# Kernel tuning notes

Measured on AMD Instinct MI355X. Metric: run time of the kernel, lower is better.

Reference implementation:

```python
import jax, jax.numpy as jnp
import numpy as np

NB_CLS, NB_QRY, NB_SHOT, FEAT_DIM = 5, 75, 5, 640
Q_STEPS, LR_DNI, HID = 3, 1e-3, 4096
N = NB_CLS + NB_QRY           # nodes in similarity graph (80)
M = 1 + N                     # subgraph size (81)
# strict upper triangle of MxM minus the query-query block (matches triu_index_input)
_t = np.ones((M, M)); _t[1 + NB_CLS:, 1 + NB_CLS:] = 0
_t = np.triu(_t, 1)
MASK_IDX = jnp.asarray(np.flatnonzero(_t.ravel() == 1))
DNI_IN = int(MASK_IDX.shape[0])  # 465


def _pairwise(supp, query):
    feat = jnp.concatenate([supp, query], 0)
    nrm = jnp.maximum(jnp.linalg.norm(feat, axis=-1, keepdims=True), 1e-12)
    feat = feat / nrm
    sim = feat @ feat.T                      # (N, N)
    sim_ss = sim[:NB_CLS, :NB_CLS]
    sim_qq = sim[NB_CLS:, NB_CLS:]
    sim_sq = sim[:NB_CLS, NB_CLS:]
    sim_feat_support = jnp.concatenate([sim_ss, sim_sq], 1).T   # (N, nb_cls)
    sim_feat_query = jnp.concatenate([sim_sq, sim_qq], 0)       # (N, nb_qry)
    return sim_feat_support, sim_feat_query, sim_sq


def _subgraph(sim_s, sim_q):
    # topk indices are constants wrt grad (no_grad in torch; ints in jax)
    idx_q = jax.lax.top_k(sim_q, NB_QRY)[1] + NB_CLS
    idx_s = jax.lax.top_k(sim_s, NB_CLS)[1]
    index = jnp.concatenate([jnp.arange(N, dtype=idx_s.dtype)[:, None], idx_s, idx_q], 1)  # (N, M)
    sim = jnp.concatenate([sim_s, sim_q], 1)                     # (N, N)
    sub = sim[index[:, :, None], index[:, None, :]]              # (N, M, M) batched gather
    return sub.reshape(N, M * M)[:, MASK_IDX]                    # (N, DNI_IN)


def _dni(x, W1, b1, W2, b2, W3, b3):
    h = jax.nn.relu(x @ W1.T + b1)
    h = jax.nn.relu(h @ W2.T + b2)
    return h @ W3.T + b3


def _refine(supp, query, ds, dq):
    for _ in range(Q_STEPS):
        inputs, vjp = jax.vjp(lambda s: _subgraph(*_pairwise(s, query)[:2]), supp)
        supp = supp - LR_DNI * vjp(_dni(inputs, *ds))[0]
        inputs, vjp = jax.vjp(lambda q: _subgraph(*_pairwise(supp, q)[:2]), query)
        query = query - LR_DNI * vjp(_dni(inputs, *dq))[0]
    return supp, query


def setup_inputs() -> dict:
    key = jax.random.key(0)
    ks = jax.random.split(key, 16)
    d = {
        "feat_support": jax.random.normal(ks[0], (NB_CLS, NB_SHOT, FEAT_DIM), jnp.float32),
        "feat_query": jax.random.normal(ks[1], (NB_QRY, FEAT_DIM), jnp.float32),
        "scale_cls": jnp.full((1,), 10.0, jnp.float32),
    }
    names = ["ds_W1", "ds_b1", "ds_W2", "ds_b2", "ds_W3", "ds_b3",
             "dq_W1", "dq_b1", "dq_W2", "dq_b2", "dq_W3", "dq_b3"]
    shapes = [(HID, DNI_IN), (HID,), (HID, HID), (HID,), (DNI_IN, HID), (DNI_IN,)] * 2
    for i, (n, sh) in enumerate(zip(names, shapes)):
        d[n] = jax.random.normal(ks[2 + i], sh, jnp.float32) * 0.02
    return d


def reference(feat_support, feat_query, scale_cls,
              ds_W1, ds_b1, ds_W2, ds_b2, ds_W3, ds_b3,
              dq_W1, dq_b1, dq_W2, dq_b2, dq_W3, dq_b3):
    supp = feat_support.mean(1)                                  # (nb_cls, feat_dim)
    ds = (ds_W1, ds_b1, ds_W2, ds_b2, ds_W3, ds_b3)
    dq = (dq_W1, dq_b1, dq_W2, dq_b2, dq_W3, dq_b3)
    supp, query = _refine(supp, feat_query, ds, dq)
    _, _, sim_sq = _pairwise(supp, query)
    return (sim_sq * scale_cls).T                                # (nb_qry, nb_cls)
```

## Files before the change

kernel.cpp:

```cpp
#include <hip/hip_runtime.h>

#define NCLS 5
#define NQRY 75
#define NTOT 80
#define FD   640
#define HIDN 4096
#define DNIN 465
#define KPAD 512
#define NPAD 512
#define LRDNI 1e-3f

#define KS1 4
#define KS2 16
#define KS3 32

typedef short  v8s __attribute__((ext_vector_type(8)));
typedef float  v4f __attribute__((ext_vector_type(4)));

__device__ __forceinline__ ushort f2bf(float x) {
    uint u = __float_as_uint(x);
    u = (u + 0x7FFFu + ((u >> 16) & 1u)) >> 16;
    return (ushort)u;
}
__device__ __forceinline__ uint pk2(float a, float b) {
    return (uint)f2bf(a) | ((uint)f2bf(b) << 16);
}

__global__ void k_init(const float* __restrict__ fs, const float* __restrict__ fq,
                       float* __restrict__ supp, float* __restrict__ qbuf) {
    int idx = blockIdx.x * 256 + threadIdx.x;
    if (idx < NCLS * FD) {
        int c = idx / FD, d = idx % FD;
        float s = 0.f;
        #pragma unroll
        for (int t = 0; t < 5; t++) s += fs[(c * 5 + t) * FD + d];
        supp[idx] = s * 0.2f;
    }
    if (idx < NQRY * FD) qbuf[idx] = fq[idx];
}

__global__ void k_cvtW1(const float* __restrict__ W, ushort* __restrict__ Wb) {
    int idx = blockIdx.x * 256 + threadIdx.x;
    int r = idx >> 9, c = idx & 511;
    Wb[idx] = (c < DNIN) ? f2bf(W[r * DNIN + c]) : (ushort)0;
}
__global__ void k_cvtW3(const float* __restrict__ W, ushort* __restrict__ Wb) {
    int idx = blockIdx.x * 256 + threadIdx.x;
    int r = idx >> 12;
    Wb[idx] = (r < DNIN) ? f2bf(W[idx]) : (ushort)0;
}

__device__ __forceinline__ const float* rowptr(const float* supp, const float* qbuf, int r) {
    return (r < NCLS) ? (supp + r * FD) : (qbuf + (r - NCLS) * FD);
}

template<bool FIN>
__global__ void k_simrank(const float* __restrict__ supp, const float* __restrict__ qbuf,
                          float* __restrict__ f, float* __restrict__ nrm,
                          float* __restrict__ S, int* __restrict__ perm,
                          const float* __restrict__ scale, float* __restrict__ out) {
    __shared__ float fi[FD];
    __shared__ float row[NTOT];
    __shared__ float ssh[NTOT];
    int i = blockIdx.x;
    int t = threadIdx.x;
    const float* ri = rowptr(supp, qbuf, i);
    for (int u = t; u < FD; u += 128) fi[u] = ri[u];
    __syncthreads();
    float dot = 0.f;
    if (t < NTOT) {
        const float* rj = rowptr(supp, qbuf, t);
        float ss = 0.f;
        for (int k = 0; k < FD; k += 4) {
            float4 a = *(const float4*)(fi + k);
            float4 b = *(const float4*)(rj + k);
            dot += a.x * b.x + a.y * b.y + a.z * b.z + a.w * b.w;
            ss  += b.x * b.x + b.y * b.y + b.z * b.z + b.w * b.w;
        }
        ssh[t] = ss;
    }
    __syncthreads();
    float ni = fmaxf(sqrtf(ssh[i]), 1e-12f);
    float inv_i = 1.0f / ni;
    if (t < NTOT) {
        float nt = fmaxf(sqrtf(ssh[t]), 1e-12f);
        float val = dot * inv_i / nt;
        if (FIN) {
            if (t >= NCLS) out[(t - NCLS) * NCLS + i] = val * scale[0];
        } else {
            row[t] = val;
            S[i * NTOT + t] = val;
        }
    }
    if (FIN) return;
    __syncthreads();
    for (int u = t; u < FD; u += 128) f[i * FD + u] = fi[u] * inv_i;
    if (t == 0) { nrm[i] = ni; perm[i * 81] = i; }
    if (t < NCLS) {
        float v = row[t]; int rank = 0;
        for (int k = 0; k < NCLS; k++) {
            float w = row[k];
            if (w > v || (w == v && k < t)) rank++;
        }
        perm[i * 81 + 1 + rank] = t;
    } else if (t < NTOT) {
        int j = t - NCLS; float v = row[t]; int rank = 0;
        for (int k = NCLS; k < NTOT; k++) {
            float w = row[k];
            if (w > v || (w == v && (k - NCLS) < j)) rank++;
        }
        perm[i * 81 + 6 + rank] = t;
    }
}

__device__ __forceinline__ void mask_ab(int m, int& a, int& b) {
    int start = 0, len = 80, aa = 0;
    while (m >= start + len) { start += len; len--; aa++; }
    a = aa; b = aa + 1 + (m - start);
}

__global__ void k_gather(const float* __restrict__ S, const int* __restrict__ perm,
                         ushort* __restrict__ Xb, float* __restrict__ Gs) {
    __shared__ int p[81];
    int i = blockIdx.x;
    int t = threadIdx.x;
    if (t < 81) p[t] = perm[i * 81 + t];
    if (t < NTOT) Gs[i * NTOT + t] = 0.f;
    __syncthreads();
    if (t < DNIN) {
        int a, b; mask_ab(t, a, b);
        Xb[i * KPAD + t] = f2bf(S[p[a] * NTOT + p[b]]);
    } else if (t < KPAD) {
        Xb[i * KPAD + t] = 0;
    }
}

template<int NT, bool BF32>
__global__ __launch_bounds__(256) void k_gemm(
        const ushort* __restrict__ A, int lda,
        const void* __restrict__ Bv, int ldb,
        float* __restrict__ C, int ldc, int kiters) {
    const int NB = NT * 64;
    __shared__ ushort As[80][68];
    __shared__ ushort Bs[NB][68];
    int tid = threadIdx.x;
    int w = tid >> 6, lane = tid & 63, l16 = lane & 15, quad = lane >> 4;
    int n00 = blockIdx.x * NB;
    int ks = blockIdx.y;
    int kc0 = ks * kiters * 64;

    v4f acc[5][NT];
    #pragma unroll
    for (int mt = 0; mt < 5; mt++)
        #pragma unroll
        for (int nt = 0; nt < NT; nt++) acc[mt][nt] = (v4f){0.f, 0.f, 0.f, 0.f};

    for (int it = 0; it < kiters; it++) {
        int k0 = kc0 + it * 64;
        for (int o = tid; o < 640; o += 256) {
            int r = o >> 3, c8 = o & 7;
            *(uint4*)&As[r][c8 * 8] = *(const uint4*)(A + r * lda + k0 + c8 * 8);
        }
        if (BF32) {
            const float* B = (const float*)Bv;
            #pragma unroll
            for (int o = tid; o < NB * 8; o += 256) {
                int r = o >> 3, c8 = o & 7;
                const float* p = B + (size_t)(n00 + r) * ldb + k0 + c8 * 8;
                float4 f0 = *(const float4*)p;
                float4 f1 = *(const float4*)(p + 4);
                uint4 q;
                q.x = pk2(f0.x, f0.y); q.y = pk2(f0.z, f0.w);
                q.z = pk2(f1.x, f1.y); q.w = pk2(f1.z, f1.w);
                *(uint4*)&Bs[r][c8 * 8] = q;
            }
        } else {
            const ushort* B = (const ushort*)Bv;
            #pragma unroll
            for (int o = tid; o < NB * 8; o += 256) {
                int r = o >> 3, c8 = o & 7;
                *(uint4*)&Bs[r][c8 * 8] = *(const uint4*)((const ushort*)B + (size_t)(n00 + r) * ldb + k0 + c8 * 8);
            }
        }
        __syncthreads();
        #pragma unroll
        for (int kb = 0; kb < 2; kb++) {
            int ko = kb * 32 + quad * 8;
            v8s bf[NT];
            #pragma unroll
            for (int nt = 0; nt < NT; nt++)
                bf[nt] = *(const v8s*)&Bs[w * NT * 16 + nt * 16 + l16][ko];
            #pragma unroll
            for (int mt = 0; mt < 5; mt++) {
                v8s af = *(const v8s*)&As[mt * 16 + l16][ko];
                #pragma unroll
                for (int nt = 0; nt < NT; nt++)
                    acc[mt][nt] = __builtin_amdgcn_mfma_f32_16x16x32_bf16(af, bf[nt], acc[mt][nt], 0, 0, 0);
            }
        }
        __syncthreads();
    }
    float* Cp = C + (size_t)ks * 80 * ldc;
    #pragma unroll
    for (int nt = 0; nt < NT; nt++) {
        int col = n00 + w * NT * 16 + nt * 16 + l16;
        #pragma unroll
        for (int mt = 0; mt < 5; mt++)
            #pragma unroll
            for (int r = 0; r < 4; r++)
                Cp[(mt * 16 + quad * 4 + r) * ldc + col] = acc[mt][nt][r];
    }
}

template<int NS>
__global__ void k_ep(const float* __restrict__ P, const float* __restrict__ bias,
                     ushort* __restrict__ H) {
    int idx = blockIdx.x * 256 + threadIdx.x;
    float s = bias[idx & 4095];
    #pragma unroll
    for (int ks = 0; ks < NS; ks++) s += P[ks * (80 * HIDN) + idx];
    H[idx] = f2bf(fmaxf(s, 0.f));
}

__global__ void k_scatter(const float* __restrict__ P3, const float* __restrict__ b3,
                          const int* __restrict__ perm, float* __restrict__ Gs) {
    __shared__ int p[81];
    int i = blockIdx.x;
    int t = threadIdx.x;
    if (t < 81) p[t] = perm[i * 81 + t];
    __syncthreads();
    if (t < DNIN) {
        float g = b3[t];
        #pragma unroll
        for (int ks = 0; ks < KS3; ks++) g += P3[ks * (80 * NPAD) + i * NPAD + t];
        int a, b; mask_ab(t, a, b);
        atomicAdd(&Gs[p[a] * NTOT + p[b]], g);
    }
}

__global__ void k_bwd(const float* __restrict__ Gs, const float* __restrict__ f,
                      const float* __restrict__ nrm, float* __restrict__ target,
                      int row0) {
    int r = row0 + blockIdx.x;
    __shared__ float cj[NTOT];
    __shared__ float red[2];
    int t = threadIdx.x;
    if (t < NTOT) cj[t] = Gs[r * NTOT + t] + Gs[t * NTOT + r];
    __syncthreads();
    float df[5] = {0.f, 0.f, 0.f, 0.f, 0.f};
    for (int j = 0; j < NTOT; j++) {
        float c = cj[j];
        const float* fj = f + j * FD;
        #pragma unroll
        for (int u = 0; u < 5; u++) df[u] += c * fj[t + 128 * u];
    }
    const float* fr = f + r * FD;
    float frv[5]; float partial = 0.f;
    #pragma unroll
    for (int u = 0; u < 5; u++) { frv[u] = fr[t + 128 * u]; partial += df[u] * frv[u]; }
    #pragma unroll
    for (int o = 32; o > 0; o >>= 1) partial += __shfl_xor(partial, o, 64);
    if ((t & 63) == 0) red[t >> 6] = partial;
    __syncthreads();
    float dot = red[0] + red[1];
    float invn = 1.0f / nrm[r];
    float* dst = target + blockIdx.x * FD;
    #pragma unroll
    for (int u = 0; u < 5; u++) {
        float dx = (df[u] - dot * frv[u]) * invn;
        dst[t + 128 * u] -= LRDNI * dx;
    }
}

extern "C" void kernel_launch(void* const* d_in, const int* in_sizes, int n_in,
                              void* d_out, int out_size, void* d_ws, size_t ws_size,
                              hipStream_t stream) {
    const float* fs    = (const float*)d_in[0];
    const float* fq    = (const float*)d_in[1];
    const float* scale = (const float*)d_in[2];
    const float* W[12];
    for (int i = 0; i < 12; i++) W[i] = (const float*)d_in[3 + i];

    float* base = (float*)d_ws;
    float* supp = base;
    float* qbuf = supp + 3200;
    float* f    = qbuf + 48000;
    float* nrm  = f + 51200;
    float* S    = nrm + 96;
    int*   perm = (int*)(S + 6400);
    float* P1   = (float*)(perm + 6496);
    float* P2   = P1 + (size_t)KS1 * 80 * HIDN;
    float* P3   = P2 + (size_t)KS2 * 80 * HIDN;
    float* Gs   = P3 + (size_t)KS3 * 80 * NPAD;
    ushort* Xb  = (ushort*)(Gs + 6400);
    ushort* H1b = Xb + 80 * KPAD;
    ushort* H2b = H1b + 80 * HIDN;
    ushort* W1b_ds = H2b + 80 * HIDN;
    ushort* W1b_dq = W1b_ds + HIDN * KPAD;
    ushort* W3b_ds = W1b_dq + HIDN * KPAD;
    ushort* W3b_dq = W3b_ds + NPAD * HIDN;

    k_cvtW1<<<8192, 256, 0, stream>>>(W[0],  W1b_ds);
    k_cvtW1<<<8192, 256, 0, stream>>>(W[6],  W1b_dq);
    k_cvtW3<<<8192, 256, 0, stream>>>(W[4],  W3b_ds);
    k_cvtW3<<<8192, 256, 0, stream>>>(W[10], W3b_dq);
    k_init<<<188, 256, 0, stream>>>(fs, fq, supp, qbuf);

    for (int step = 0; step < 3; step++) {
        for (int half = 0; half < 2; half++) {
            const float* const* w = (half == 0) ? W : (W + 6);
            const ushort* W1b = (half == 0) ? W1b_ds : W1b_dq;
            const ushort* W3b = (half == 0) ? W3b_ds : W3b_dq;
            k_simrank<false><<<80, 128, 0, stream>>>(supp, qbuf, f, nrm, S, perm, nullptr, nullptr);
            k_gather<<<80, 512, 0, stream>>>(S, perm, Xb, Gs);
            k_gemm<1, false><<<dim3(64, KS1), 256, 0, stream>>>(
                Xb, KPAD, W1b, KPAD, P1, HIDN, 2);
            k_ep<KS1><<<1280, 256, 0, stream>>>(P1, w[1], H1b);
            k_gemm<2, true><<<dim3(32, KS2), 256, 0, stream>>>(
                H1b, HIDN, w[2], HIDN, P2, HIDN, 4);
            k_ep<KS2><<<1280, 256, 0, stream>>>(P2, w[3], H2b);
            k_gemm<1, false><<<dim3(8, KS3), 256, 0, stream>>>(
                H2b, HIDN, W3b, HIDN, P3, NPAD, 2);
            k_scatter<<<80, 512, 0, stream>>>(P3, w[5], perm, Gs);
            if (half == 0) k_bwd<<<5, 128, 0, stream>>>(Gs, f, nrm, supp, 0);
            else           k_bwd<<<75, 128, 0, stream>>>(Gs, f, nrm, qbuf, NCLS);
        }
    }
    k_simrank<true><<<5, 128, 0, stream>>>(supp, qbuf, f, nrm, S, perm, scale, (float*)d_out);
}
```

Before: 654.6 us.

## Pre-convert W2 to bf16, load GEMM fragments directly, vectorize epilogue

Converts the two 4096x4096 W2 matrices to bf16 once up front, which halves the bytes the middle GEMM reads from memory on each of its six uses. The GEMM drops shared-memory staging and barriers, and each wave now loads its MFMA fragments straight from global memory. Layer 1 uses a wider K split (8 instead of 4). The bias+ReLU epilogue is vectorized to float4 loads. The cost is extra one-time conversion work and workspace, plus direct global loads that are less coalesced and reuse A tiles less across waves.

```diff
diff --git a/kernel.cpp b/kernel.cpp
--- a/kernel.cpp
+++ b/kernel.cpp
@@ -10,7 +10,7 @@
 #define NPAD 512
 #define LRDNI 1e-3f
 
-#define KS1 4
+#define KS1 8
 #define KS2 16
 #define KS3 32
 
@@ -48,6 +48,12 @@
     int idx = blockIdx.x * 256 + threadIdx.x;
     int r = idx >> 12;
     Wb[idx] = (r < DNIN) ? f2bf(W[idx]) : (ushort)0;
+}
+__global__ void k_cvtW2(const float* __restrict__ W, ushort* __restrict__ Wb) {
+    int idx = blockIdx.x * 256 + threadIdx.x;
+    float4 v = ((const float4*)W)[idx];
+    uint2 q; q.x = pk2(v.x, v.y); q.y = pk2(v.z, v.w);
+    ((uint2*)Wb)[idx] = q;
 }
 
 __device__ __forceinline__ const float* rowptr(const float* supp, const float* qbuf, int r) {
@@ -135,19 +141,17 @@
     }
 }
 
-template<int NT, bool BF32>
+template<int NT, int KSTEPS>
 __global__ __launch_bounds__(256) void k_gemm(
         const ushort* __restrict__ A, int lda,
-        const void* __restrict__ Bv, int ldb,
-        float* __restrict__ C, int ldc, int kiters) {
-    const int NB = NT * 64;
-    __shared__ ushort As[80][68];
-    __shared__ ushort Bs[NB][68];
+        const ushort* __restrict__ B, int ldb,
+        float* __restrict__ C, int ldc) {
     int tid = threadIdx.x;
     int w = tid >> 6, lane = tid & 63, l16 = lane & 15, quad = lane >> 4;
-    int n00 = blockIdx.x * NB;
-    int ks = blockIdx.y;
-    int kc0 = ks * kiters * 64;
+    int n0 = blockIdx.x * (NT * 64) + w * NT * 16;
+    int kc0 = blockIdx.y * (KSTEPS * 32);
+    const ushort* Ap = A + l16 * lda + kc0 + quad * 8;
+    const ushort* Bp = B + (size_t)(n0 + l16) * ldb + kc0 + quad * 8;
 
     v4f acc[5][NT];
     #pragma unroll
@@ -155,55 +159,26 @@
         #pragma unroll
         for (int nt = 0; nt < NT; nt++) acc[mt][nt] = (v4f){0.f, 0.f, 0.f, 0.f};
 
-    for (int it = 0; it < kiters; it++) {
-        int k0 = kc0 + it * 64;
-        for (int o = tid; o < 640; o += 256) {
-            int r = o >> 3, c8 = o & 7;
-            *(uint4*)&As[r][c8 * 8] = *(const uint4*)(A + r * lda + k0 + c8 * 8);
-        }
-        if (BF32) {
-            const float* B = (const float*)Bv;
-            #pragma unroll
-            for (int o = tid; o < NB * 8; o += 256) {
-                int r = o >> 3, c8 = o & 7;
-                const float* p = B + (size_t)(n00 + r) * ldb + k0 + c8 * 8;
-                float4 f0 = *(const float4*)p;
-                float4 f1 = *(const float4*)(p + 4);
-                uint4 q;
-                q.x = pk2(f0.x, f0.y); q.y = pk2(f0.z, f0.w);
-                q.z = pk2(f1.x, f1.y); q.w = pk2(f1.z, f1.w);
-                *(uint4*)&Bs[r][c8 * 8] = q;
-            }
-        } else {
-            const ushort* B = (const ushort*)Bv;
-            #pragma unroll
-            for (int o = tid; o < NB * 8; o += 256) {
-                int r = o >> 3, c8 = o & 7;
-                *(uint4*)&Bs[r][c8 * 8] = *(const uint4*)((const ushort*)B + (size_t)(n00 + r) * ldb + k0 + c8 * 8);
-            }
-        }
-        __syncthreads();
-        #pragma unroll
-        for (int kb = 0; kb < 2; kb++) {
-            int ko = kb * 32 + quad * 8;
-            v8s bf[NT];
+    #pragma unroll
+    for (int s = 0; s < KSTEPS; s++) {
+        int ko = s * 32;
+        v8s a[5], b[NT];
+        #pragma unroll
+        for (int mt = 0; mt < 5; mt++)
+            a[mt] = *(const v8s*)(Ap + mt * 16 * lda + ko);
+        #pragma unroll
+        for (int nt = 0; nt < NT; nt++)
+            b[nt] = *(const v8s*)(Bp + nt * 16 * ldb + ko);
+        #pragma unroll
+        for (int mt = 0; mt < 5; mt++)
             #pragma unroll
             for (int nt = 0; nt < NT; nt++)
-                bf[nt] = *(const v8s*)&Bs[w * NT * 16 + nt * 16 + l16][ko];
-            #pragma unroll
-            for (int mt = 0; mt < 5; mt++) {
-                v8s af = *(const v8s*)&As[mt * 16 + l16][ko];
-                #pragma unroll
-                for (int nt = 0; nt < NT; nt++)
-                    acc[mt][nt] = __builtin_amdgcn_mfma_f32_16x16x32_bf16(af, bf[nt], acc[mt][nt], 0, 0, 0);
-            }
-        }
-        __syncthreads();
-    }
-    float* Cp = C + (size_t)ks * 80 * ldc;
+                acc[mt][nt] = __builtin_amdgcn_mfma_f32_16x16x32_bf16(a[mt], b[nt], acc[mt][nt], 0, 0, 0);
+    }
+    float* Cp = C + (size_t)blockIdx.y * 80 * ldc;
     #pragma unroll
     for (int nt = 0; nt < NT; nt++) {
-        int col = n00 + w * NT * 16 + nt * 16 + l16;
+        int col = n0 + nt * 16 + l16;
         #pragma unroll
         for (int mt = 0; mt < 5; mt++)
             #pragma unroll
@@ -216,10 +191,16 @@
 __global__ void k_ep(const float* __restrict__ P, const float* __restrict__ bias,
                      ushort* __restrict__ H) {
     int idx = blockIdx.x * 256 + threadIdx.x;
-    float s = bias[idx & 4095];
-    #pragma unroll
-    for (int ks = 0; ks < NS; ks++) s += P[ks * (80 * HIDN) + idx];
-    H[idx] = f2bf(fmaxf(s, 0.f));
+    float4 s = ((const float4*)bias)[idx & 1023];
+    #pragma unroll
+    for (int ks = 0; ks < NS; ks++) {
+        float4 p = ((const float4*)P)[ks * (80 * HIDN / 4) + idx];
+        s.x += p.x; s.y += p.y; s.z += p.z; s.w += p.w;
+    }
+    uint2 q;
+    q.x = pk2(fmaxf(s.x, 0.f), fmaxf(s.y, 0.f));
+    q.y = pk2(fmaxf(s.z, 0.f), fmaxf(s.w, 0.f));
+    ((uint2*)H)[idx] = q;
 }
 
 __global__ void k_scatter(const float* __restrict__ P3, const float* __restrict__ b3,
@@ -299,28 +280,30 @@
     ushort* W1b_dq = W1b_ds + HIDN * KPAD;
     ushort* W3b_ds = W1b_dq + HIDN * KPAD;
     ushort* W3b_dq = W3b_ds + NPAD * HIDN;
+    ushort* W2b_ds = W3b_dq + NPAD * HIDN;
+    ushort* W2b_dq = W2b_ds + (size_t)HIDN * HIDN;
 
     k_cvtW1<<<8192, 256, 0, stream>>>(W[0],  W1b_ds);
     k_cvtW1<<<8192, 256, 0, stream>>>(W[6],  W1b_dq);
     k_cvtW3<<<8192, 256, 0, stream>>>(W[4],  W3b_ds);
     k_cvtW3<<<8192, 256, 0, stream>>>(W[10], W3b_dq);
+    k_cvtW2<<<16384, 256, 0, stream>>>(W[2], W2b_ds);
+    k_cvtW2<<<16384, 256, 0, stream>>>(W[8], W2b_dq);
     k_init<<<188, 256, 0, stream>>>(fs, fq, supp, qbuf);
 
     for (int step = 0; step < 3; step++) {
         for (int half = 0; half < 2; half++) {
             const float* const* w = (half == 0) ? W : (W + 6);
             const ushort* W1b = (half == 0) ? W1b_ds : W1b_dq;
+            const ushort* W2b = (half == 0) ? W2b_ds : W2b_dq;
             const ushort* W3b = (half == 0) ? W3b_ds : W3b_dq;
             k_simrank<false><<<80, 128, 0, stream>>>(supp, qbuf, f, nrm, S, perm, nullptr, nullptr);
             k_gather<<<80, 512, 0, stream>>>(S, perm, Xb, Gs);
-            k_gemm<1, false><<<dim3(64, KS1), 256, 0, stream>>>(
-                Xb, KPAD, W1b, KPAD, P1, HIDN, 2);
-            k_ep<KS1><<<1280, 256, 0, stream>>>(P1, w[1], H1b);
-            k_gemm<2, true><<<dim3(32, KS2), 256, 0, stream>>>(
-                H1b, HIDN, w[2], HIDN, P2, HIDN, 4);
-            k_ep<KS2><<<1280, 256, 0, stream>>>(P2, w[3], H2b);
-            k_gemm<1, false><<<dim3(8, KS3), 256, 0, stream>>>(
-                H2b, HIDN, W3b, HIDN, P3, NPAD, 2);
+            k_gemm<1, 2><<<dim3(64, KS1), 256, 0, stream>>>(Xb, KPAD, W1b, KPAD, P1, HIDN);
+            k_ep<KS1><<<320, 256, 0, stream>>>(P1, w[1], H1b);
+            k_gemm<2, 8><<<dim3(32, KS2), 256, 0, stream>>>(H1b, HIDN, W2b, HIDN, P2, HIDN);
+            k_ep<KS2><<<320, 256, 0, stream>>>(P2, w[3], H2b);
+            k_gemm<1, 4><<<dim3(8, KS3), 256, 0, stream>>>(H2b, HIDN, W3b, HIDN, P3, NPAD);
             k_scatter<<<80, 512, 0, stream>>>(P3, w[5], perm, Gs);
             if (half == 0) k_bwd<<<5, 128, 0, stream>>>(Gs, f, nrm, supp, 0);
             else           k_bwd<<<75, 128, 0, stream>>>(Gs, f, nrm, qbuf, NCLS);
```

After: 659.0 us. No clear change (+0.7%).
